# Performance work log

Hardware: AMD Instinct MI355X
Metric: run time of the kernel (lower is better)

Reference implementation:

```python
import jax, jax.numpy as jnp
import numpy as np

NUM_HEADS = 16
HIDDEN = 1024
EPS = 1e-5


def _layer_norm(x, g, b):
    m = jnp.mean(x, axis=-1, keepdims=True)
    v = jnp.mean(jnp.square(x - m), axis=-1, keepdims=True)
    return (x - m) * jax.lax.rsqrt(v + EPS) * g + b


def setup_inputs() -> dict:
    key = jax.random.key(0)
    ks = jax.random.split(key, 6)
    B, S, H = 2, 2048, HIDDEN
    x = jax.random.normal(ks[0], (B, S, H), dtype=jnp.float32)
    # True = masked (original passes ~attn_mask to SDPA); causal mask
    causal = ~jnp.tril(jnp.ones((S, S), dtype=bool))
    attn_mask = causal[None, None, :, :]  # [1,1,S,S]
    sc = 1.0 / np.sqrt(H)
    qkv_w = jax.random.normal(ks[1], (H, 3 * H), dtype=jnp.float32) * sc
    qkv_b = jnp.zeros((3 * H,), dtype=jnp.float32)
    out_w = jax.random.normal(ks[2], (H, H), dtype=jnp.float32) * sc
    out_b = jnp.zeros((H,), dtype=jnp.float32)
    w1 = jax.random.normal(ks[3], (H, 4 * H), dtype=jnp.float32) * sc
    b1 = jnp.zeros((4 * H,), dtype=jnp.float32)
    w2 = jax.random.normal(ks[4], (4 * H, H), dtype=jnp.float32) * (1.0 / np.sqrt(4 * H))
    b2 = jnp.zeros((H,), dtype=jnp.float32)
    return {
        'x': x, 'attn_mask': attn_mask,
        'qkv_w': qkv_w, 'qkv_b': qkv_b, 'out_w': out_w, 'out_b': out_b,
        'w1': w1, 'b1': b1, 'w2': w2, 'b2': b2,
        'ln1_g': jnp.ones((H,), jnp.float32), 'ln1_b': jnp.zeros((H,), jnp.float32),
        'ln2_g': jnp.ones((H,), jnp.float32), 'ln2_b': jnp.zeros((H,), jnp.float32),
    }


def reference(x, attn_mask, qkv_w, qkv_b, out_w, out_b, w1, b1, w2, b2,
              ln1_g, ln1_b, ln2_g, ln2_b):
    B, S, H = x.shape
    nh = NUM_HEADS
    hd = H // nh
    qkv = x @ qkv_w + qkv_b                      # [B,S,3H]
    q, k, v = jnp.split(qkv, 3, axis=-1)
    q = q.reshape(B, S, nh, hd).transpose(0, 2, 1, 3)  # [B,nh,S,hd]
    k = k.reshape(B, S, nh, hd).transpose(0, 2, 1, 3)
    v = v.reshape(B, S, nh, hd).transpose(0, 2, 1, 3)
    scores = jnp.einsum('bhqd,bhkd->bhqk', q, k) / jnp.sqrt(jnp.asarray(hd, x.dtype))
    scores = jnp.where(attn_mask, jnp.finfo(scores.dtype).min, scores)
    p = jax.nn.softmax(scores, axis=-1)
    attn = jnp.einsum('bhqk,bhkd->bhqd', p, v)   # [B,nh,S,hd]
    attn = attn.transpose(0, 2, 1, 3).reshape(B, S, H)
    attn = attn @ out_w + out_b
    x = _layer_norm(x + attn, ln1_g, ln1_b)
    h = jax.nn.relu(x @ w1 + b1) @ w2 + b2
    x = _layer_norm(x + h, ln2_g, ln2_b)
    return x
```

## Files before the change

kernel.cpp:

```cpp
#include <hip/hip_runtime.h>
#include <hip/hip_bf16.h>

typedef __bf16 bf16x8 __attribute__((ext_vector_type(8)));
typedef __bf16 bf16x4 __attribute__((ext_vector_type(4)));
typedef float f32x4 __attribute__((ext_vector_type(4)));

__device__ __forceinline__ void gload16(void* lds, const void* g) {
  __builtin_amdgcn_global_load_lds((const __attribute__((address_space(1))) void*)g,
                                   (__attribute__((address_space(3))) void*)lds, 16, 0, 0);
}

__global__ __launch_bounds__(256)
void transpose_cast(const float* __restrict__ in, __bf16* __restrict__ out, int R, int C)
{
  __shared__ __bf16 tile[32][33];
  const int bc = blockIdx.x * 32, br = blockIdx.y * 32;
  const int lx = threadIdx.x & 31, ly = threadIdx.x >> 5;
#pragma unroll
  for (int p = 0; p < 4; ++p)
    tile[ly + p * 8][lx] = (__bf16)in[(size_t)(br + ly + p * 8) * C + bc + lx];
  __syncthreads();
#pragma unroll
  for (int p = 0; p < 4; ++p)
    out[(size_t)(bc + ly + p * 8) * R + br + lx] = tile[lx][ly + p * 8];
}

__global__ __launch_bounds__(256)
void vtrans(const __bf16* __restrict__ qkv, __bf16* __restrict__ vtg)
{
  __shared__ __bf16 tile[32][33];
  const int sx = blockIdx.x * 32;
  const int dy = blockIdx.y * 32;
  const int z = blockIdx.z;
  const int b = z >> 4, h = z & 15;
  const int lx = threadIdx.x & 31, ly = threadIdx.x >> 5;
  const __bf16* src = qkv + (size_t)b * 2048 * 3072 + 2048 + h * 64;
#pragma unroll
  for (int p = 0; p < 4; ++p)
    tile[ly + p * 8][lx] = src[(size_t)(sx + ly + p * 8) * 3072 + dy + lx];
  __syncthreads();
  __bf16* dst = vtg + (size_t)z * 64 * 2048;
#pragma unroll
  for (int p = 0; p < 4; ++p)
    dst[(size_t)(dy + ly + p * 8) * 2048 + sx + lx] = tile[lx][ly + p * 8];
}

__global__ __launch_bounds__(256)
void cast_bf16(const float* __restrict__ in, __bf16* __restrict__ out)
{
  const int i = (blockIdx.x * 256 + threadIdx.x) * 4;
  float4 v = *(const float4*)(in + i);
  out[i] = (__bf16)v.x; out[i + 1] = (__bf16)v.y;
  out[i + 2] = (__bf16)v.z; out[i + 3] = (__bf16)v.w;
}

template<int BN, int BK, bool OUT_BF16, bool RELU, bool RESID, bool RBF16, bool SPLIT>
__global__ __launch_bounds__(256)
void gemm_bt(const __bf16* __restrict__ A, const __bf16* __restrict__ Bt,
             const float* __restrict__ bias, const void* __restrict__ residv,
             void* __restrict__ C0v, float* __restrict__ C1,
             int M, int N, int Kfull, int Ksub)
{
  constexpr int NW = BN / 32;
  constexpr int CH = BK / 8;
  __shared__ __bf16 As[2][128 * BK];
  __shared__ __bf16 Bs[2][BN * BK];
  const int tid = threadIdx.x;
  const int wave = tid >> 6, lane = tid & 63;
  const int g = lane >> 4, l16 = lane & 15;
  const int row0 = blockIdx.x * 128, col0 = blockIdx.y * BN;
  const int z = SPLIT ? blockIdx.z : 0;
  const __bf16* Az = A + (size_t)z * Ksub;
  const __bf16* Bz = Bt + (size_t)z * Ksub;
  const int wr = wave >> 1, wc = wave & 1;
  f32x4 acc[4][NW] = {};
  const int nk = Ksub / BK;

  auto KEY = [](int row) -> int { return (BK == 64) ? (row & 7) : ((row >> 1) & 3); };

  auto STAGE = [&](int buf, int k0) {
#pragma unroll
    for (int r = 0; r < 128 * CH / 256; ++r) {
      const int seg = r * 256 + tid;
      const int row = seg / CH, cp = seg % CH;
      const int src = (cp ^ KEY(row)) * 8;
      gload16(&As[buf][(r * 256 + wave * 64) * 8], &Az[(size_t)(row0 + row) * Kfull + k0 + src]);
    }
#pragma unroll
    for (int r = 0; r < BN * CH / 256; ++r) {
      const int seg = r * 256 + tid;
      const int row = seg / CH, cp = seg % CH;
      const int src = (cp ^ KEY(row)) * 8;
      gload16(&Bs[buf][(r * 256 + wave * 64) * 8], &Bz[(size_t)(col0 + row) * Kfull + k0 + src]);
    }
  };

  STAGE(0, 0);
  __syncthreads();
  int cur = 0;
  for (int t = 0; t < nk; ++t) {
    if (t + 1 < nk) STAGE(cur ^ 1, (t + 1) * BK);
#pragma unroll
    for (int kk = 0; kk < BK / 32; ++kk) {
      bf16x8 af[4], bfr[NW];
#pragma unroll
      for (int m = 0; m < 4; ++m) {
        const int row = wr * 64 + m * 16 + l16;
        af[m] = *(const bf16x8*)&As[cur][row * BK + (((kk * 4 + g) ^ KEY(row)) << 3)];
      }
#pragma unroll
      for (int n = 0; n < NW; ++n) {
        const int row = wc * (BN / 2) + n * 16 + l16;
        bfr[n] = *(const bf16x8*)&Bs[cur][row * BK + (((kk * 4 + g) ^ KEY(row)) << 3)];
      }
#pragma unroll
      for (int m = 0; m < 4; ++m)
#pragma unroll
        for (int n = 0; n < NW; ++n)
          acc[m][n] = __builtin_amdgcn_mfma_f32_16x16x32_bf16(af[m], bfr[n], acc[m][n], 0, 0, 0);
    }
    __syncthreads();
    cur ^= 1;
  }
#pragma unroll
  for (int n = 0; n < NW; ++n) {
    const int col = col0 + wc * (BN / 2) + n * 16 + l16;
    float bv = 0.f;
    if (!SPLIT || z == 0) bv = bias[col];
#pragma unroll
    for (int m = 0; m < 4; ++m) {
      const int rrow = row0 + wr * 64 + m * 16 + g * 4;
#pragma unroll
      for (int r = 0; r < 4; ++r) {
        float v = acc[m][n][r] + bv;
        const size_t idx = (size_t)(rrow + r) * N + col;
        if (RESID && (!SPLIT || z == 0)) {
          if (RBF16) v += (float)((const __bf16*)residv)[idx];
          else       v += ((const float*)residv)[idx];
        }
        if (SPLIT) {
          float* C = z ? C1 : (float*)C0v;
          C[idx] = v;
        } else {
          if (RELU)  v = fmaxf(v, 0.f);
          if (OUT_BF16) ((__bf16*)C0v)[idx] = (__bf16)v;
          else          ((float*)C0v)[idx] = v;
        }
      }
    }
  }
}

__global__ __launch_bounds__(256)
void attn_fwd(const __bf16* __restrict__ qkv, const __bf16* __restrict__ vtg,
              __bf16* __restrict__ ctx)
{
  constexpr int S = 2048, H = 1024, W3 = 3 * H;
  __shared__ __bf16 Ks[2][64 * 64];
  __shared__ __bf16 Vt[2][64 * 64];
  __shared__ __bf16 Ps[4][16 * 64];
  const int tid = threadIdx.x, wave = tid >> 6, lane = tid & 63;
  const int g = lane >> 4, l16 = lane & 15;
  const int perm = ((l16 & 7) << 1) | (l16 >> 3);
  const int bh = blockIdx.x;
  const int b = bh >> 4, h = bh & 15;
  const size_t base = (size_t)b * S * W3;
  const __bf16* Qg = qkv + base;
  const __bf16* Kg = qkv + base + H;
  const __bf16* Vg = vtg + (size_t)bh * 64 * S;

  auto STAGE_KV = [&](int buf, int kv0) {
#pragma unroll
    for (int r = 0; r < 2; ++r) {
      const int seg = r * 256 + tid;
      const int row = seg >> 3;
      const int ko = ((seg & 7) ^ (row & 7)) * 8;
      gload16(&Ks[buf][(r * 256 + wave * 64) * 8], &Kg[(size_t)(kv0 + row) * W3 + h * 64 + ko]);
      gload16(&Vt[buf][(r * 256 + wave * 64) * 8], &Vg[(size_t)row * S + kv0 + ko]);
    }
  };

#pragma unroll 1
  for (int half = 0; half < 2; ++half) {
    const int qi = half ? (31 - blockIdx.y) : blockIdx.y;
    const int q0 = qi * 64;
    const int qrow = q0 + wave * 16 + l16;
    bf16x8 qa[2];
#pragma unroll
    for (int kk = 0; kk < 2; ++kk)
      qa[kk] = *(const bf16x8*)&Qg[(size_t)qrow * W3 + h * 64 + kk * 32 + g * 8];

    f32x4 o[4] = {};
    float lsum = 0.f;
    const int nT = qi + 1;

    STAGE_KV(0, 0);
    __syncthreads();
    int cur = 0;

    for (int t = 0; t < nT; ++t) {
      const int kv0 = t * 64;
      if (t + 1 < nT) STAGE_KV(cur ^ 1, kv0 + 64);

      f32x4 s[4] = {};
      __builtin_amdgcn_s_setprio(1);
#pragma unroll
      for (int kk = 0; kk < 2; ++kk) {
        bf16x8 kb[4];
#pragma unroll
        for (int n = 0; n < 4; ++n) {
          const int row = n * 16 + l16;
          kb[n] = *(const bf16x8*)&Ks[cur][row * 64 + ((kk * 32 + g * 8) ^ ((row & 7) << 3))];
        }
#pragma unroll
        for (int n = 0; n < 4; ++n)
          s[n] = __builtin_amdgcn_mfma_f32_16x16x32_bf16(kb[n], qa[kk], s[n], 0, 0, 0);
      }
      __builtin_amdgcn_s_setprio(0);

      const bool diag = (t == nT - 1);
#pragma unroll
      for (int n = 0; n < 4; ++n) {
        float lp[4];
#pragma unroll
        for (int r = 0; r < 4; ++r) {
          const int ka = kv0 + n * 16 + g * 4 + r;
          float p = exp2f(s[n][r] * 0.18033688f);
          if (diag && ka > qrow) p = 0.f;
          lp[r] = p;
          lsum += p;
        }
        bf16x4 pk;
        pk[0] = (__bf16)lp[0]; pk[1] = (__bf16)lp[1];
        pk[2] = (__bf16)lp[2]; pk[3] = (__bf16)lp[3];
        *(bf16x4*)&Ps[wave][l16 * 64 + (((4 * n + g) ^ perm) << 2)] = pk;
      }

      __builtin_amdgcn_s_setprio(1);
#pragma unroll
      for (int kk = 0; kk < 2; ++kk) {
        const int hb = 8 * kk + 2 * g;
        bf16x4 p0 = *(const bf16x4*)&Ps[wave][l16 * 64 + ((hb ^ perm) << 2)];
        bf16x4 p1 = *(const bf16x4*)&Ps[wave][l16 * 64 + (((hb + 1) ^ perm) << 2)];
        bf16x8 pa = __builtin_shufflevector(p0, p1, 0, 1, 2, 3, 4, 5, 6, 7);
        bf16x8 vb[4];
#pragma unroll
        for (int n2 = 0; n2 < 4; ++n2) {
          const int row = n2 * 16 + l16;
          vb[n2] = *(const bf16x8*)&Vt[cur][row * 64 + ((kk * 32 + g * 8) ^ ((row & 7) << 3))];
        }
#pragma unroll
        for (int n2 = 0; n2 < 4; ++n2)
          o[n2] = __builtin_amdgcn_mfma_f32_16x16x32_bf16(pa, vb[n2], o[n2], 0, 0, 0);
      }
      __builtin_amdgcn_s_setprio(0);
      __syncthreads();
      cur ^= 1;
    }

    lsum += __shfl_xor(lsum, 16);
    lsum += __shfl_xor(lsum, 32);
#pragma unroll
    for (int r = 0; r < 4; ++r) {
      const float den = __shfl(lsum, g * 4 + r);
      const float inv = 1.f / den;
      const int qr = q0 + wave * 16 + g * 4 + r;
#pragma unroll
      for (int n2 = 0; n2 < 4; ++n2) {
        const int d = n2 * 16 + l16;
        ctx[(size_t)(b * S + qr) * H + h * 64 + d] = (__bf16)(o[n2][r] * inv);
      }
    }
  }
}

template<bool WRITE_F32, bool WRITE_BF16, bool TWO_IN>
__global__ __launch_bounds__(256)
void ln_kernel(const float* __restrict__ in, const float* __restrict__ in2,
               const float* __restrict__ gw, const float* __restrict__ bw,
               float* __restrict__ outf, __bf16* __restrict__ outb)
{
  const int row = blockIdx.x, tid = threadIdx.x;
  float4 xv = ((const float4*)(in + (size_t)row * 1024))[tid];
  if (TWO_IN) {
    const float4 yv = ((const float4*)(in2 + (size_t)row * 1024))[tid];
    xv.x += yv.x; xv.y += yv.y; xv.z += yv.z; xv.w += yv.w;
  }
  float s = xv.x + xv.y + xv.z + xv.w;
  float s2 = xv.x * xv.x + xv.y * xv.y + xv.z * xv.z + xv.w * xv.w;
#pragma unroll
  for (int off = 32; off; off >>= 1) { s += __shfl_xor(s, off); s2 += __shfl_xor(s2, off); }
  __shared__ float ps[8];
  if ((tid & 63) == 0) { ps[tid >> 6] = s; ps[4 + (tid >> 6)] = s2; }
  __syncthreads();
  s = ps[0] + ps[1] + ps[2] + ps[3];
  s2 = ps[4] + ps[5] + ps[6] + ps[7];
  const float mean = s * (1.f / 1024.f);
  const float var = s2 * (1.f / 1024.f) - mean * mean;
  const float rs = rsqrtf(var + 1e-5f);
  const float4 gv = ((const float4*)gw)[tid];
  const float4 bv = ((const float4*)bw)[tid];
  float4 y;
  y.x = (xv.x - mean) * rs * gv.x + bv.x;
  y.y = (xv.y - mean) * rs * gv.y + bv.y;
  y.z = (xv.z - mean) * rs * gv.z + bv.z;
  y.w = (xv.w - mean) * rs * gv.w + bv.w;
  if (WRITE_F32)
    ((float4*)(outf + (size_t)row * 1024))[tid] = y;
  if (WRITE_BF16) {
    __bf16* ob = outb + (size_t)row * 1024 + tid * 4;
    ob[0] = (__bf16)y.x; ob[1] = (__bf16)y.y; ob[2] = (__bf16)y.z; ob[3] = (__bf16)y.w;
  }
}

extern "C" void kernel_launch(void* const* d_in, const int* in_sizes, int n_in,
                              void* d_out, int out_size, void* d_ws, size_t ws_size,
                              hipStream_t stream)
{
  (void)in_sizes; (void)n_in; (void)out_size; (void)ws_size;
  const float* x     = (const float*)d_in[0];
  const float* qkv_w = (const float*)d_in[2];
  const float* qkv_b = (const float*)d_in[3];
  const float* out_w = (const float*)d_in[4];
  const float* out_b = (const float*)d_in[5];
  const float* w1    = (const float*)d_in[6];
  const float* b1    = (const float*)d_in[7];
  const float* w2    = (const float*)d_in[8];
  const float* b2    = (const float*)d_in[9];
  const float* ln1g  = (const float*)d_in[10];
  const float* ln1b  = (const float*)d_in[11];
  const float* ln2g  = (const float*)d_in[12];
  const float* ln2b  = (const float*)d_in[13];

  char* ws = (char*)d_ws;
  __bf16* wt_qkv = (__bf16*)(ws + 0);
  __bf16* wt_out = (__bf16*)(ws + 6291456);
  __bf16* wt_w1  = (__bf16*)(ws + 8388608);
  __bf16* wt_w2  = (__bf16*)(ws + 16777216);
  __bf16* xb     = (__bf16*)(ws + 25165824);
  __bf16* big    = (__bf16*)(ws + 33554432);
  float*  res    = (float*)(ws + 67108864);
  __bf16* x1b    = (__bf16*)(ws + 100663296);
  __bf16* vtg    = (__bf16*)res;
  float*  qB     = (float*)ws;

  transpose_cast<<<dim3(96, 32), 256, 0, stream>>>(qkv_w, wt_qkv, 1024, 3072);
  transpose_cast<<<dim3(32, 32), 256, 0, stream>>>(out_w, wt_out, 1024, 1024);
  transpose_cast<<<dim3(128, 32), 256, 0, stream>>>(w1, wt_w1, 1024, 4096);
  transpose_cast<<<dim3(32, 128), 256, 0, stream>>>(w2, wt_w2, 4096, 1024);
  cast_bf16<<<4096, 256, 0, stream>>>(x, xb);

  gemm_bt<128, 64, true, false, false, false, false><<<dim3(32, 24), 256, 0, stream>>>(
      xb, wt_qkv, qkv_b, nullptr, big, nullptr, 4096, 3072, 1024, 1024);
  vtrans<<<dim3(64, 2, 32), 256, 0, stream>>>(big, vtg);
  attn_fwd<<<dim3(32, 16), 256, 0, stream>>>(big, vtg, xb);
  gemm_bt<64, 64, false, false, true, false, false><<<dim3(32, 16), 256, 0, stream>>>(
      xb, wt_out, out_b, x, res, nullptr, 4096, 1024, 1024, 1024);
  ln_kernel<false, true, false><<<4096, 256, 0, stream>>>(res, nullptr, ln1g, ln1b,
                                                          nullptr, x1b);
  gemm_bt<128, 64, true, true, false, false, false><<<dim3(32, 32), 256, 0, stream>>>(
      x1b, wt_w1, b1, nullptr, big, nullptr, 4096, 4096, 1024, 1024);
  gemm_bt<128, 64, false, false, true, true, true><<<dim3(32, 8, 2), 256, 0, stream>>>(
      big, wt_w2, b2, x1b, res, qB, 4096, 1024, 4096, 2048);
  ln_kernel<true, false, true><<<4096, 256, 0, stream>>>(res, qB, ln2g, ln2b,
                                                         (float*)d_out, nullptr);
}
```

Baseline: 233.8 us.

## Merge weight transposes, split attention q-tiles across blocks, store split-K partials in bf16

Merges the four weight transpose-cast launches into a single launch that dispatches on block index. Attention stops having each block walk two paired q-tiles in sequence; it launches one block per q-tile, ordered heaviest first, to raise parallelism and shorten the tail. The split-K FC2 partials are written as bf16 and summed in a new LN kernel, which halves partial traffic but rounds pre-norm sums to bf16 and may cost accuracy.

```diff
diff --git a/kernel.cpp b/kernel.cpp
--- a/kernel.cpp
+++ b/kernel.cpp
@@ -11,10 +11,19 @@
 }
 
 __global__ __launch_bounds__(256)
-void transpose_cast(const float* __restrict__ in, __bf16* __restrict__ out, int R, int C)
+void transpose4(const float* __restrict__ s0, __bf16* __restrict__ d0,
+                const float* __restrict__ s1, __bf16* __restrict__ d1,
+                const float* __restrict__ s2, __bf16* __restrict__ d2,
+                const float* __restrict__ s3, __bf16* __restrict__ d3)
 {
   __shared__ __bf16 tile[32][33];
-  const int bc = blockIdx.x * 32, br = blockIdx.y * 32;
+  int id = blockIdx.x;
+  const float* in; __bf16* out; int R, C, bx, by;
+  if (id < 3072)      { in = s0; out = d0; R = 1024; C = 3072; bx = id % 96;  by = id / 96; }
+  else if (id < 4096) { id -= 3072; in = s1; out = d1; R = 1024; C = 1024; bx = id % 32;  by = id / 32; }
+  else if (id < 8192) { id -= 4096; in = s2; out = d2; R = 1024; C = 4096; bx = id % 128; by = id / 128; }
+  else                { id -= 8192; in = s3; out = d3; R = 4096; C = 1024; bx = id % 32;  by = id / 32; }
+  const int bc = bx * 32, br = by * 32;
   const int lx = threadIdx.x & 31, ly = threadIdx.x >> 5;
 #pragma unroll
   for (int p = 0; p < 4; ++p)
@@ -58,7 +67,7 @@
 __global__ __launch_bounds__(256)
 void gemm_bt(const __bf16* __restrict__ A, const __bf16* __restrict__ Bt,
              const float* __restrict__ bias, const void* __restrict__ residv,
-             void* __restrict__ C0v, float* __restrict__ C1,
+             void* __restrict__ C0v, void* __restrict__ C1v,
              int M, int N, int Kfull, int Ksub)
 {
   constexpr int NW = BN / 32;
@@ -139,8 +148,7 @@
           else       v += ((const float*)residv)[idx];
         }
         if (SPLIT) {
-          float* C = z ? C1 : (float*)C0v;
-          C[idx] = v;
+          ((__bf16*)(z ? C1v : C0v))[idx] = (__bf16)v;
         } else {
           if (RELU)  v = fmaxf(v, 0.f);
           if (OUT_BF16) ((__bf16*)C0v)[idx] = (__bf16)v;
@@ -163,6 +171,8 @@
   const int g = lane >> 4, l16 = lane & 15;
   const int perm = ((l16 & 7) << 1) | (l16 >> 3);
   const int bh = blockIdx.x;
+  const int y = blockIdx.y, j = y & 7, m = y >> 3;
+  const int qi = (m == 0) ? (31 - j) : (m == 1) ? (16 + j) : (m == 2) ? (15 - j) : j;
   const int b = bh >> 4, h = bh & 15;
   const size_t base = (size_t)b * S * W3;
   const __bf16* Qg = qkv + base;
@@ -180,112 +190,104 @@
     }
   };
 
-#pragma unroll 1
-  for (int half = 0; half < 2; ++half) {
-    const int qi = half ? (31 - blockIdx.y) : blockIdx.y;
-    const int q0 = qi * 64;
-    const int qrow = q0 + wave * 16 + l16;
-    bf16x8 qa[2];
-#pragma unroll
-    for (int kk = 0; kk < 2; ++kk)
-      qa[kk] = *(const bf16x8*)&Qg[(size_t)qrow * W3 + h * 64 + kk * 32 + g * 8];
-
-    f32x4 o[4] = {};
-    float lsum = 0.f;
-    const int nT = qi + 1;
-
-    STAGE_KV(0, 0);
+  const int q0 = qi * 64;
+  const int qrow = q0 + wave * 16 + l16;
+  bf16x8 qa[2];
+#pragma unroll
+  for (int kk = 0; kk < 2; ++kk)
+    qa[kk] = *(const bf16x8*)&Qg[(size_t)qrow * W3 + h * 64 + kk * 32 + g * 8];
+
+  f32x4 o[4] = {};
+  float lsum = 0.f;
+  const int nT = qi + 1;
+
+  STAGE_KV(0, 0);
+  __syncthreads();
+  int cur = 0;
+
+  for (int t = 0; t < nT; ++t) {
+    const int kv0 = t * 64;
+    if (t + 1 < nT) STAGE_KV(cur ^ 1, kv0 + 64);
+
+    f32x4 s[4] = {};
+    __builtin_amdgcn_s_setprio(1);
+#pragma unroll
+    for (int kk = 0; kk < 2; ++kk) {
+      bf16x8 kb[4];
+#pragma unroll
+      for (int n = 0; n < 4; ++n) {
+        const int row = n * 16 + l16;
+        kb[n] = *(const bf16x8*)&Ks[cur][row * 64 + ((kk * 32 + g * 8) ^ ((row & 7) << 3))];
+      }
+#pragma unroll
+      for (int n = 0; n < 4; ++n)
+        s[n] = __builtin_amdgcn_mfma_f32_16x16x32_bf16(kb[n], qa[kk], s[n], 0, 0, 0);
+    }
+    __builtin_amdgcn_s_setprio(0);
+
+    const bool diag = (t == nT - 1);
+#pragma unroll
+    for (int n = 0; n < 4; ++n) {
+      float lp[4];
+#pragma unroll
+      for (int r = 0; r < 4; ++r) {
+        const int ka = kv0 + n * 16 + g * 4 + r;
+        float p = exp2f(s[n][r] * 0.18033688f);
+        if (diag && ka > qrow) p = 0.f;
+        lp[r] = p;
+        lsum += p;
+      }
+      bf16x4 pk;
+      pk[0] = (__bf16)lp[0]; pk[1] = (__bf16)lp[1];
+      pk[2] = (__bf16)lp[2]; pk[3] = (__bf16)lp[3];
+      *(bf16x4*)&Ps[wave][l16 * 64 + (((4 * n + g) ^ perm) << 2)] = pk;
+    }
+
+    __builtin_amdgcn_s_setprio(1);
+#pragma unroll
+    for (int kk = 0; kk < 2; ++kk) {
+      const int hb = 8 * kk + 2 * g;
+      bf16x4 p0 = *(const bf16x4*)&Ps[wave][l16 * 64 + ((hb ^ perm) << 2)];
+      bf16x4 p1 = *(const bf16x4*)&Ps[wave][l16 * 64 + (((hb + 1) ^ perm) << 2)];
+      bf16x8 pa = __builtin_shufflevector(p0, p1, 0, 1, 2, 3, 4, 5, 6, 7);
+      bf16x8 vb[4];
+#pragma unroll
+      for (int n2 = 0; n2 < 4; ++n2) {
+        const int row = n2 * 16 + l16;
+        vb[n2] = *(const bf16x8*)&Vt[cur][row * 64 + ((kk * 32 + g * 8) ^ ((row & 7) << 3))];
+      }
+#pragma unroll
+      for (int n2 = 0; n2 < 4; ++n2)
+        o[n2] = __builtin_amdgcn_mfma_f32_16x16x32_bf16(pa, vb[n2], o[n2], 0, 0, 0);
+    }
+    __builtin_amdgcn_s_setprio(0);
     __syncthreads();
-    int cur = 0;
-
-    for (int t = 0; t < nT; ++t) {
-      const int kv0 = t * 64;
-      if (t + 1 < nT) STAGE_KV(cur ^ 1, kv0 + 64);
-
-      f32x4 s[4] = {};
-      __builtin_amdgcn_s_setprio(1);
-#pragma unroll
-      for (int kk = 0; kk < 2; ++kk) {
-        bf16x8 kb[4];
-#pragma unroll
-        for (int n = 0; n < 4; ++n) {
-          const int row = n * 16 + l16;
-          kb[n] = *(const bf16x8*)&Ks[cur][row * 64 + ((kk * 32 + g * 8) ^ ((row & 7) << 3))];
-        }
-#pragma unroll
-        for (int n = 0; n < 4; ++n)
-          s[n] = __builtin_amdgcn_mfma_f32_16x16x32_bf16(kb[n], qa[kk], s[n], 0, 0, 0);
-      }
-      __builtin_amdgcn_s_setprio(0);
-
-      const bool diag = (t == nT - 1);
-#pragma unroll
-      for (int n = 0; n < 4; ++n) {
-        float lp[4];
-#pragma unroll
-        for (int r = 0; r < 4; ++r) {
-          const int ka = kv0 + n * 16 + g * 4 + r;
-          float p = exp2f(s[n][r] * 0.18033688f);
-          if (diag && ka > qrow) p = 0.f;
-          lp[r] = p;
-          lsum += p;
-        }
-        bf16x4 pk;
-        pk[0] = (__bf16)lp[0]; pk[1] = (__bf16)lp[1];
-        pk[2] = (__bf16)lp[2]; pk[3] = (__bf16)lp[3];
-        *(bf16x4*)&Ps[wave][l16 * 64 + (((4 * n + g) ^ perm) << 2)] = pk;
-      }
-
-      __builtin_amdgcn_s_setprio(1);
-#pragma unroll
-      for (int kk = 0; kk < 2; ++kk) {
-        const int hb = 8 * kk + 2 * g;
-        bf16x4 p0 = *(const bf16x4*)&Ps[wave][l16 * 64 + ((hb ^ perm) << 2)];
-        bf16x4 p1 = *(const bf16x4*)&Ps[wave][l16 * 64 + (((hb + 1) ^ perm) << 2)];
-        bf16x8 pa = __builtin_shufflevector(p0, p1, 0, 1, 2, 3, 4, 5, 6, 7);
-        bf16x8 vb[4];
-#pragma unroll
-        for (int n2 = 0; n2 < 4; ++n2) {
-          const int row = n2 * 16 + l16;
-          vb[n2] = *(const bf16x8*)&Vt[cur][row * 64 + ((kk * 32 + g * 8) ^ ((row & 7) << 3))];
-        }
-#pragma unroll
-        for (int n2 = 0; n2 < 4; ++n2)
-          o[n2] = __builtin_amdgcn_mfma_f32_16x16x32_bf16(pa, vb[n2], o[n2], 0, 0, 0);
-      }
-      __builtin_amdgcn_s_setprio(0);
-      __syncthreads();
-      cur ^= 1;
-    }
-
-    lsum += __shfl_xor(lsum, 16);
-    lsum += __shfl_xor(lsum, 32);
-#pragma unroll
-    for (int r = 0; r < 4; ++r) {
-      const float den = __shfl(lsum, g * 4 + r);
-      const float inv = 1.f / den;
-      const int qr = q0 + wave * 16 + g * 4 + r;
-#pragma unroll
-      for (int n2 = 0; n2 < 4; ++n2) {
-        const int d = n2 * 16 + l16;
-        ctx[(size_t)(b * S + qr) * H + h * 64 + d] = (__bf16)(o[n2][r] * inv);
-      }
-    }
+    cur ^= 1;
   }
-}
-
-template<bool WRITE_F32, bool WRITE_BF16, bool TWO_IN>
-__global__ __launch_bounds__(256)
-void ln_kernel(const float* __restrict__ in, const float* __restrict__ in2,
+
+  lsum += __shfl_xor(lsum, 16);
+  lsum += __shfl_xor(lsum, 32);
+#pragma unroll
+  for (int r = 0; r < 4; ++r) {
+    const float den = __shfl(lsum, g * 4 + r);
+    const float inv = 1.f / den;
+    const int qr = q0 + wave * 16 + g * 4 + r;
+#pragma unroll
+    for (int n2 = 0; n2 < 4; ++n2) {
+      const int d = n2 * 16 + l16;
+      ctx[(size_t)(b * S + qr) * H + h * 64 + d] = (__bf16)(o[n2][r] * inv);
+    }
+  }
+}
+
+template<bool WRITE_F32, bool WRITE_BF16>
+__global__ __launch_bounds__(256)
+void ln_kernel(const float* __restrict__ in,
                const float* __restrict__ gw, const float* __restrict__ bw,
                float* __restrict__ outf, __bf16* __restrict__ outb)
 {
   const int row = blockIdx.x, tid = threadIdx.x;
   float4 xv = ((const float4*)(in + (size_t)row * 1024))[tid];
-  if (TWO_IN) {
-    const float4 yv = ((const float4*)(in2 + (size_t)row * 1024))[tid];
-    xv.x += yv.x; xv.y += yv.y; xv.z += yv.z; xv.w += yv.w;
-  }
   float s = xv.x + xv.y + xv.z + xv.w;
   float s2 = xv.x * xv.x + xv.y * xv.y + xv.z * xv.z + xv.w * xv.w;
 #pragma unroll
@@ -313,6 +315,41 @@
   }
 }
 
+__global__ __launch_bounds__(256)
+void ln2b_kernel(const __bf16* __restrict__ in, const __bf16* __restrict__ in2,
+                 const float* __restrict__ gw, const float* __restrict__ bw,
+                 float* __restrict__ outf)
+{
+  const int row = blockIdx.x, tid = threadIdx.x;
+  const bf16x4 a = ((const bf16x4*)(in + (size_t)row * 1024))[tid];
+  const bf16x4 b = ((const bf16x4*)(in2 + (size_t)row * 1024))[tid];
+  float4 xv;
+  xv.x = (float)a[0] + (float)b[0];
+  xv.y = (float)a[1] + (float)b[1];
+  xv.z = (float)a[2] + (float)b[2];
+  xv.w = (float)a[3] + (float)b[3];
+  float s = xv.x + xv.y + xv.z + xv.w;
+  float s2 = xv.x * xv.x + xv.y * xv.y + xv.z * xv.z + xv.w * xv.w;
+#pragma unroll
+  for (int off = 32; off; off >>= 1) { s += __shfl_xor(s, off); s2 += __shfl_xor(s2, off); }
+  __shared__ float ps[8];
+  if ((tid & 63) == 0) { ps[tid >> 6] = s; ps[4 + (tid >> 6)] = s2; }
+  __syncthreads();
+  s = ps[0] + ps[1] + ps[2] + ps[3];
+  s2 = ps[4] + ps[5] + ps[6] + ps[7];
+  const float mean = s * (1.f / 1024.f);
+  const float var = s2 * (1.f / 1024.f) - mean * mean;
+  const float rs = rsqrtf(var + 1e-5f);
+  const float4 gv = ((const float4*)gw)[tid];
+  const float4 bv = ((const float4*)bw)[tid];
+  float4 y;
+  y.x = (xv.x - mean) * rs * gv.x + bv.x;
+  y.y = (xv.y - mean) * rs * gv.y + bv.y;
+  y.z = (xv.z - mean) * rs * gv.z + bv.z;
+  y.w = (xv.w - mean) * rs * gv.w + bv.w;
+  ((float4*)(outf + (size_t)row * 1024))[tid] = y;
+}
+
 extern "C" void kernel_launch(void* const* d_in, const int* in_sizes, int n_in,
                               void* d_out, int out_size, void* d_ws, size_t ws_size,
                               hipStream_t stream)
@@ -342,26 +379,22 @@
   float*  res    = (float*)(ws + 67108864);
   __bf16* x1b    = (__bf16*)(ws + 100663296);
   __bf16* vtg    = (__bf16*)res;
-  float*  qB     = (float*)ws;
-
-  transpose_cast<<<dim3(96, 32), 256, 0, stream>>>(qkv_w, wt_qkv, 1024, 3072);
-  transpose_cast<<<dim3(32, 32), 256, 0, stream>>>(out_w, wt_out, 1024, 1024);
-  transpose_cast<<<dim3(128, 32), 256, 0, stream>>>(w1, wt_w1, 1024, 4096);
-  transpose_cast<<<dim3(32, 128), 256, 0, stream>>>(w2, wt_w2, 4096, 1024);
+  __bf16* pz0    = (__bf16*)res;
+  __bf16* pz1    = (__bf16*)ws;
+
+  transpose4<<<12288, 256, 0, stream>>>(qkv_w, wt_qkv, out_w, wt_out, w1, wt_w1, w2, wt_w2);
   cast_bf16<<<4096, 256, 0, stream>>>(x, xb);
 
   gemm_bt<128, 64, true, false, false, false, false><<<dim3(32, 24), 256, 0, stream>>>(
       xb, wt_qkv, qkv_b, nullptr, big, nullptr, 4096, 3072, 1024, 1024);
   vtrans<<<dim3(64, 2, 32), 256, 0, stream>>>(big, vtg);
-  attn_fwd<<<dim3(32, 16), 256, 0, stream>>>(big, vtg, xb);
+  attn_fwd<<<dim3(32, 32), 256, 0, stream>>>(big, vtg, xb);
   gemm_bt<64, 64, false, false, true, false, false><<<dim3(32, 16), 256, 0, stream>>>(
       xb, wt_out, out_b, x, res, nullptr, 4096, 1024, 1024, 1024);
-  ln_kernel<false, true, false><<<4096, 256, 0, stream>>>(res, nullptr, ln1g, ln1b,
-                                                          nullptr, x1b);
+  ln_kernel<false, true><<<4096, 256, 0, stream>>>(res, ln1g, ln1b, nullptr, x1b);
   gemm_bt<128, 64, true, true, false, false, false><<<dim3(32, 32), 256, 0, stream>>>(
       x1b, wt_w1, b1, nullptr, big, nullptr, 4096, 4096, 1024, 1024);
   gemm_bt<128, 64, false, false, true, true, true><<<dim3(32, 8, 2), 256, 0, stream>>>(
-      big, wt_w2, b2, x1b, res, qB, 4096, 1024, 4096, 2048);
-  ln_kernel<true, false, true><<<4096, 256, 0, stream>>>(res, qB, ln2g, ln2b,
-                                                         (float*)d_out, nullptr);
-}
+      big, wt_w2, b2, x1b, pz0, pz1, 4096, 1024, 4096, 2048);
+  ln2b_kernel<<<4096, 256, 0, stream>>>(pz0, pz1, ln2g, ln2b, (float*)d_out);
+}
```

After: 223.1 us. 1.05x faster.
